# Optimization experiments

Hardware: AMD Instinct MI355X
Metric: run time of the kernel (lower is better)

Reference implementation:

```python
import jax, jax.numpy as jnp
import numpy as np

CLAMP_MIN, CLAMP_MAX = -3.0, 3.0
RANK = 16


def setup_inputs() -> dict:
    key = jax.random.key(0)
    ks = jax.random.split(key, 8)
    B, N, D, H, R = 8, 4096, 1024, 256, RANK
    s = 0.02  # small weight std so clamp/exp are well-conditioned
    return {
        "query_emb": jax.random.normal(ks[0], (B, D), jnp.float32),
        "context_embs": jax.random.normal(ks[1], (B, N, D), jnp.float32),
        "W1": jax.random.normal(ks[2], (D, H), jnp.float32) * s,
        "b1": jnp.zeros((H,), jnp.float32),
        "Wd": jax.random.normal(ks[3], (H, D), jnp.float32) * s,
        "bd": jnp.zeros((D,), jnp.float32),
        "WL": jax.random.normal(ks[4], (H, D * R), jnp.float32) * s,
        "bL": jnp.zeros((D * R,), jnp.float32),
        "Wdel": jax.random.normal(ks[5], (H, D), jnp.float32) * s,
        "bdel": jnp.zeros((D,), jnp.float32),
        "Wa": jax.random.normal(ks[6], (H, D), jnp.float32) * s,
        "ba": jnp.zeros((D,), jnp.float32),
    }


def reference(query_emb, context_embs, W1, b1, Wd, bd, WL, bL, Wdel, bdel, Wa, ba):
    B, N, D = context_embs.shape
    R = RANK
    # Backbone: Linear + ReLU (assumed MLP backbone)
    h = jax.nn.relu(query_emb @ W1 + b1)                      # (B,H)
    # Parameter heads (SkewGaussian.forward)
    log_d = jnp.clip(h @ Wd + bd, CLAMP_MIN, CLAMP_MAX)       # (B,D)
    L = (h @ WL + bL).reshape(B, D, R) * 0.1                  # (B,D,R)
    delta = (h @ Wdel + bdel) * 0.1                           # (B,D)
    alpha = h @ Wa + ba                                       # (B,D)

    mu = query_emb + delta                                    # (B,D)
    diff = context_embs - mu[:, None, :]                      # (B,N,D)
    d_inv = jnp.exp(-log_d)                                   # (B,D)

    # Diagonal Mahalanobis term
    mahal_diag = jnp.einsum('bnd,bd->bn', diff * diff, d_inv) # (B,N)

    # Woodbury correction with small RxR system per batch
    DinvL = d_inv[:, :, None] * L                             # (B,D,R)
    M = jnp.eye(R, dtype=L.dtype)[None] + jnp.einsum('bdr,bds->brs', L, DinvL)  # (B,R,R)
    M_inv = jnp.linalg.inv(M)
    v = diff * d_inv[:, None, :]                              # (B,N,D)
    w = jnp.einsum('bdr,bnd->brn', L, v)                      # (B,R,N)
    correction = jnp.sum(w * jnp.einsum('brs,bsn->brn', M_inv, w), axis=1)  # (B,N)

    mahal = mahal_diag - correction
    log_det = jnp.sum(log_d, axis=-1, keepdims=True) + jnp.linalg.slogdet(M)[1][:, None]  # (B,1)
    symmetric_score = -0.5 * (mahal + log_det)                # (B,N)

    skew_input = jnp.einsum('bd,bnd->bn', alpha, diff)
    skew_score = jax.nn.log_sigmoid(skew_input)
    return symmetric_score + skew_score
```

## Files before the change

### kernel.cpp

```cpp
#include <hip/hip_runtime.h>
#include <math.h>

#define BB 8
#define NN 4096
#define DD 1024
#define HH 256
#define RR 16

#define WS_GT      0
#define WS_MU      131072
#define WS_DINV    139264
#define WS_ALPHA   147456
#define WS_HP      155648
#define WS_LDP     163840
#define WS_M       163968
#define WS_MINV    166016
#define WS_LOGDET  168064
#define WS_L       168080

__global__ __launch_bounds__(256) void ka1_h(
    const float* __restrict__ qe, const float* __restrict__ W1, float* __restrict__ ws)
{
    const int b = blockIdx.x >> 2;
    const int sl = blockIdx.x & 3;
    const int c = threadIdx.x;
    __shared__ float qe_s[256];
    qe_s[c] = qe[b * DD + sl * 256 + c];
    __syncthreads();
    float a0 = 0.f, a1 = 0.f, a2 = 0.f, a3 = 0.f;
    const float* W1p = W1 + (sl * 256) * HH;
    for (int dl = 0; dl < 256; dl += 4) {
        a0 = fmaf(qe_s[dl + 0], W1p[(dl + 0) * HH + c], a0);
        a1 = fmaf(qe_s[dl + 1], W1p[(dl + 1) * HH + c], a1);
        a2 = fmaf(qe_s[dl + 2], W1p[(dl + 2) * HH + c], a2);
        a3 = fmaf(qe_s[dl + 3], W1p[(dl + 3) * HH + c], a3);
    }
    ws[WS_HP + (b * 4 + sl) * HH + c] = (a0 + a1) + (a2 + a3);
}

__global__ __launch_bounds__(256) void ka2_heads(
    const float* __restrict__ qe, const float* __restrict__ b1,
    const float* __restrict__ Wd, const float* __restrict__ bd,
    const float* __restrict__ WL, const float* __restrict__ bL,
    const float* __restrict__ Wdel, const float* __restrict__ bdel,
    const float* __restrict__ Wa, const float* __restrict__ ba,
    float* __restrict__ ws)
{
    __shared__ float h_s[BB * HH];
    __shared__ float red[4][512];
    const int tid = threadIdx.x;

    for (int i = tid; i < BB * HH; i += 256) {
        const int bb = i >> 8, c = i & 255;
        const float v = ws[WS_HP + (bb * 4 + 0) * HH + c] + ws[WS_HP + (bb * 4 + 1) * HH + c]
                      + ws[WS_HP + (bb * 4 + 2) * HH + c] + ws[WS_HP + (bb * 4 + 3) * HH + c]
                      + b1[c];
        h_s[i] = fmaxf(v, 0.f);
    }
    __syncthreads();

    const int blk = blockIdx.x;
    const int lane = tid & 63;
    const int u = tid >> 6;

    int mode; const float* W; const float* bias; int base;
    if (blk < 16)       { mode = 0; W = Wd;   bias = bd;   base = 0;  }
    else if (blk < 32)  { mode = 1; W = Wdel; bias = bdel; base = 16; }
    else if (blk < 48)  { mode = 2; W = Wa;   bias = ba;   base = 32; }
    else                { mode = 3; W = WL;   bias = bL;   base = 48; }
    const int ld = (mode == 3) ? (DD * RR) : DD;
    const int cc = (blk - base) * 64 + lane;

    float acc[8];
    #pragma unroll
    for (int b = 0; b < 8; ++b) acc[b] = 0.f;

    #pragma unroll 4
    for (int rr = 0; rr < 64; ++rr) {
        const int r = u * 64 + rr;
        const float wv = W[r * ld + cc];
        #pragma unroll
        for (int b = 0; b < 8; ++b) acc[b] = fmaf(h_s[b * HH + r], wv, acc[b]);
    }
    #pragma unroll
    for (int b = 0; b < 8; ++b) red[u][lane * 8 + b] = acc[b];
    __syncthreads();

    for (int e = tid; e < 512; e += 256) {
        const int cl = e >> 3, bb = e & 7;
        const int cm = (blk - base) * 64 + cl;
        float s = red[0][e] + red[1][e] + red[2][e] + red[3][e] + bias[cm];
        if (mode == 0) {
            const float ldv = fminf(fmaxf(s, -3.f), 3.f);
            ws[WS_DINV + bb * DD + cm] = expf(-ldv);
            red[0][e] = ldv;
        } else if (mode == 1) {
            ws[WS_MU + bb * DD + cm] = qe[bb * DD + cm] + 0.1f * s;
        } else if (mode == 2) {
            ws[WS_ALPHA + bb * DD + cm] = s;
        } else {
            ws[WS_L + bb * (DD * RR) + cm] = 0.1f * s;
        }
    }
    if (mode == 0) {
        __syncthreads();
        if (tid < 8) {
            float s = 0.f;
            for (int cl = 0; cl < 64; ++cl) s += red[0][cl * 8 + tid];
            ws[WS_LDP + blk * 8 + tid] = s;
        }
    }
}

__global__ __launch_bounds__(256) void kg_gt(float* __restrict__ ws)
{
    const int idx = blockIdx.x * 256 + threadIdx.x;
    const int d = idx & (DD - 1);
    const int r = (idx >> 10) & (RR - 1);
    const int b = idx >> 14;
    ws[WS_GT + idx] = ws[WS_DINV + b * DD + d] * ws[WS_L + (b * DD + d) * RR + r];
}

__global__ __launch_bounds__(256) void kM(float* __restrict__ ws)
{
    const int b = blockIdx.x >> 4;
    const int g = blockIdx.x & 15;
    const int tid = threadIdx.x;
    const int s = tid & 15, dg = tid >> 4;

    const float* Gt = ws + WS_GT + (size_t)b * (RR * DD) + g * DD;
    const float* Lp = ws + WS_L + (size_t)b * (DD * RR);

    float acc = 0.f;
    #pragma unroll 4
    for (int k = 0; k < 64; ++k) {
        const int d = dg * 64 + k;
        acc = fmaf(Gt[d], Lp[d * 16 + s], acc);
    }
    __shared__ float red2[16][17];
    red2[dg][s] = acc;
    __syncthreads();
    if (tid < 16) {
        float m = (tid == g) ? 1.f : 0.f;
        #pragma unroll
        for (int d2 = 0; d2 < 16; ++d2) m += red2[d2][tid];
        ws[WS_M + b * 256 + g * 16 + tid] = m;
    }
}

__global__ __launch_bounds__(256) void kGJ(float* __restrict__ ws)
{
    const int b = blockIdx.x;
    const int tid = threadIdx.x;
    const int i = tid >> 4, j = tid & 15;
    __shared__ float A[16][33];

    A[i][j] = ws[WS_M + b * 256 + i * 16 + j];
    A[i][j + 16] = (i == j) ? 1.f : 0.f;
    __syncthreads();

    float logdetM = 0.f;
    for (int k = 0; k < 16; ++k) {
        const float piv = A[k][k];
        if (tid == 0) logdetM += logf(piv);
        __syncthreads();
        if (i == k) {
            const float rinv = 1.f / piv;
            A[i][j] *= rinv;
            A[i][j + 16] *= rinv;
        }
        __syncthreads();
        const float f = (i == k) ? 0.f : A[i][k];
        __syncthreads();
        if (i != k) {
            A[i][j]      = fmaf(-f, A[k][j],      A[i][j]);
            A[i][j + 16] = fmaf(-f, A[k][j + 16], A[i][j + 16]);
        }
        __syncthreads();
    }
    ws[WS_MINV + b * 256 + i * 16 + j] = A[i][j + 16];
    if (tid == 0) {
        float lds = 0.f;
        for (int k = 0; k < 16; ++k) lds += ws[WS_LDP + k * 8 + b];
        ws[WS_LOGDET + b] = lds + logdetM;
    }
}

__global__ __launch_bounds__(512, 4) void kc_main(
    const float* __restrict__ ctx, const float* __restrict__ ws, float* __restrict__ out)
{
    const int bid = blockIdx.x;
    const int b = bid >> 7;
    const int tile = bid & 127;
    const int wave = threadIdx.x >> 6;
    const int lane = threadIdx.x & 63;
    const int n0 = tile * 32 + wave * 4;

    __shared__ float gt_s[RR * DD];
    {
        float4* gs4 = (float4*)gt_s;
        const float4* Gt4g = (const float4*)(ws + WS_GT + (size_t)b * (RR * DD));
        for (int i = threadIdx.x; i < RR * DD / 4; i += 512) gs4[i] = Gt4g[i];
    }
    __syncthreads();
    const float4* gs4 = (const float4*)gt_s;

    const float4* mu4 = (const float4*)(ws + WS_MU + b * DD);
    const float4* dv4 = (const float4*)(ws + WS_DINV + b * DD);
    const float4* al4 = (const float4*)(ws + WS_ALPHA + b * DD);
    const float4* ctx4 = (const float4*)(ctx + ((size_t)(b * NN + n0)) * DD);

    float g[4][16];
    float md[4], aa[4];
    #pragma unroll
    for (int i = 0; i < 4; ++i) {
        md[i] = 0.f; aa[i] = 0.f;
        #pragma unroll
        for (int r = 0; r < 16; ++r) g[i][r] = 0.f;
    }

    #pragma unroll
    for (int step = 0; step < 4; ++step) {
        const int fi = step * 64 + lane;
        const float4 mv = mu4[fi], dvv = dv4[fi], av = al4[fi];
        const float4 c0 = ctx4[0 * (DD / 4) + fi];
        const float4 c1 = ctx4[1 * (DD / 4) + fi];
        const float4 c2 = ctx4[2 * (DD / 4) + fi];
        const float4 c3 = ctx4[3 * (DD / 4) + fi];

        float diff[4][4];
        diff[0][0] = c0.x - mv.x; diff[0][1] = c0.y - mv.y; diff[0][2] = c0.z - mv.z; diff[0][3] = c0.w - mv.w;
        diff[1][0] = c1.x - mv.x; diff[1][1] = c1.y - mv.y; diff[1][2] = c1.z - mv.z; diff[1][3] = c1.w - mv.w;
        diff[2][0] = c2.x - mv.x; diff[2][1] = c2.y - mv.y; diff[2][2] = c2.z - mv.z; diff[2][3] = c2.w - mv.w;
        diff[3][0] = c3.x - mv.x; diff[3][1] = c3.y - mv.y; diff[3][2] = c3.z - mv.z; diff[3][3] = c3.w - mv.w;

        const float dva[4] = {dvv.x, dvv.y, dvv.z, dvv.w};
        const float ava[4] = {av.x, av.y, av.z, av.w};
        #pragma unroll
        for (int i = 0; i < 4; ++i) {
            #pragma unroll
            for (int j = 0; j < 4; ++j) {
                md[i] = fmaf(diff[i][j] * dva[j], diff[i][j], md[i]);
                aa[i] = fmaf(ava[j], diff[i][j], aa[i]);
            }
        }

        #pragma unroll
        for (int r = 0; r < 16; ++r) {
            const float4 gt = gs4[r * 256 + fi];
            #pragma unroll
            for (int i = 0; i < 4; ++i) {
                g[i][r] = fmaf(gt.x, diff[i][0], g[i][r]);
                g[i][r] = fmaf(gt.y, diff[i][1], g[i][r]);
                g[i][r] = fmaf(gt.z, diff[i][2], g[i][r]);
                g[i][r] = fmaf(gt.w, diff[i][3], g[i][r]);
            }
        }
    }

    float v[64];
    #pragma unroll
    for (int i = 0; i < 4; ++i)
        #pragma unroll
        for (int r = 0; r < 16; ++r) v[i * 16 + r] = g[i][r];

    #pragma unroll
    for (int s6 = 0; s6 < 6; ++s6) {
        const int m = 1 << s6;
        const int half = 32 >> s6;
        const bool up = (lane & m) != 0;
        #pragma unroll
        for (int ii = 0; ii < half; ++ii) {
            float x0 = v[2 * ii], x1 = v[2 * ii + 1];
            float y0 = __shfl_xor(x0, m, 64);
            float y1 = __shfl_xor(x1, m, 64);
            v[ii] = up ? (x1 + y1) : (x0 + y0);
        }
    }
    const float w = v[0];

    #pragma unroll
    for (int m = 1; m < 64; m <<= 1) {
        #pragma unroll
        for (int i = 0; i < 4; ++i) {
            md[i] += __shfl_xor(md[i], m, 64);
            aa[i] += __shfl_xor(aa[i], m, 64);
        }
    }

    const int r = lane & 15;
    const int rowbase = lane & 48;
    const float* Minv = ws + WS_MINV + b * 256 + r * 16;
    float y = 0.f;
    #pragma unroll
    for (int s = 0; s < 16; ++s) y = fmaf(Minv[s], __shfl(w, rowbase + s, 64), y);
    float corr = w * y;
    corr += __shfl_xor(corr, 1, 64);
    corr += __shfl_xor(corr, 2, 64);
    corr += __shfl_xor(corr, 4, 64);
    corr += __shfl_xor(corr, 8, 64);

    const float ld = ws[WS_LOGDET + b];
    if ((lane & 15) == 0) {
        const int i = lane >> 4;
        const float mdv = (i & 2) ? ((i & 1) ? md[3] : md[2]) : ((i & 1) ? md[1] : md[0]);
        const float aav = (i & 2) ? ((i & 1) ? aa[3] : aa[2]) : ((i & 1) ? aa[1] : aa[0]);
        const float lsig = fminf(aav, 0.f) - log1pf(expf(-fabsf(aav)));
        out[(size_t)b * NN + n0 + i] = -0.5f * (mdv - corr + ld) + lsig;
    }
}

extern "C" void kernel_launch(void* const* d_in, const int* in_sizes, int n_in,
                              void* d_out, int out_size, void* d_ws, size_t ws_size,
                              hipStream_t stream)
{
    const float* qe   = (const float*)d_in[0];
    const float* ctx  = (const float*)d_in[1];
    const float* W1   = (const float*)d_in[2];
    const float* b1   = (const float*)d_in[3];
    const float* Wd   = (const float*)d_in[4];
    const float* bd   = (const float*)d_in[5];
    const float* WL   = (const float*)d_in[6];
    const float* bL   = (const float*)d_in[7];
    const float* Wdel = (const float*)d_in[8];
    const float* bdel = (const float*)d_in[9];
    const float* Wa   = (const float*)d_in[10];
    const float* ba   = (const float*)d_in[11];
    float* out = (float*)d_out;
    float* ws  = (float*)d_ws;

    ka1_h<<<32, 256, 0, stream>>>(qe, W1, ws);
    ka2_heads<<<304, 256, 0, stream>>>(qe, b1, Wd, bd, WL, bL, Wdel, bdel, Wa, ba, ws);
    kg_gt<<<512, 256, 0, stream>>>(ws);
    kM<<<128, 256, 0, stream>>>(ws);
    kGJ<<<8, 256, 0, stream>>>(ws);
    kc_main<<<1024, 512, 0, stream>>>(ctx, ws, out);
}
```

Before: 326.2 us.

## Split W1 GEMV finer, fuse M build with Gauss-Jordan, relax main kernel occupancy

Spreads the backbone GEMV across 128 blocks instead of 32 by splitting the input dimension into 16 slices, so each block does less serial work. Merges the M-matrix reduction and the Gauss-Jordan inversion into one 1024-thread kernel per batch, removing a launch and a global round trip. The main context kernel drops its occupancy hint from 4 to 2 blocks per CU, partially unrolls the step loop, and defers the d_inv/alpha loads to shorten register live ranges. The fused kernel runs only 8 blocks doing serial loops, and lower occupancy in the bandwidth-bound main kernel could hurt latency hiding.

```diff
diff --git a/kernel.cpp b/kernel.cpp
--- a/kernel.cpp
+++ b/kernel.cpp
@@ -12,30 +12,30 @@
 #define WS_DINV    139264
 #define WS_ALPHA   147456
 #define WS_HP      155648
-#define WS_LDP     163840
-#define WS_M       163968
-#define WS_MINV    166016
-#define WS_LOGDET  168064
-#define WS_L       168080
+#define WS_LDP     188416
+#define WS_MINV    188544
+#define WS_LOGDET  190592
+#define WS_L       190608
 
 __global__ __launch_bounds__(256) void ka1_h(
     const float* __restrict__ qe, const float* __restrict__ W1, float* __restrict__ ws)
 {
-    const int b = blockIdx.x >> 2;
-    const int sl = blockIdx.x & 3;
+    const int b = blockIdx.x >> 4;
+    const int sl = blockIdx.x & 15;
     const int c = threadIdx.x;
-    __shared__ float qe_s[256];
-    qe_s[c] = qe[b * DD + sl * 256 + c];
+    __shared__ float qe_s[64];
+    if (c < 64) qe_s[c] = qe[b * DD + sl * 64 + c];
     __syncthreads();
     float a0 = 0.f, a1 = 0.f, a2 = 0.f, a3 = 0.f;
-    const float* W1p = W1 + (sl * 256) * HH;
-    for (int dl = 0; dl < 256; dl += 4) {
+    const float* W1p = W1 + (sl * 64) * HH;
+    #pragma unroll 4
+    for (int dl = 0; dl < 64; dl += 4) {
         a0 = fmaf(qe_s[dl + 0], W1p[(dl + 0) * HH + c], a0);
         a1 = fmaf(qe_s[dl + 1], W1p[(dl + 1) * HH + c], a1);
         a2 = fmaf(qe_s[dl + 2], W1p[(dl + 2) * HH + c], a2);
         a3 = fmaf(qe_s[dl + 3], W1p[(dl + 3) * HH + c], a3);
     }
-    ws[WS_HP + (b * 4 + sl) * HH + c] = (a0 + a1) + (a2 + a3);
+    ws[WS_HP + (b * 16 + sl) * HH + c] = (a0 + a1) + (a2 + a3);
 }
 
 __global__ __launch_bounds__(256) void ka2_heads(
@@ -52,9 +52,9 @@
 
     for (int i = tid; i < BB * HH; i += 256) {
         const int bb = i >> 8, c = i & 255;
-        const float v = ws[WS_HP + (bb * 4 + 0) * HH + c] + ws[WS_HP + (bb * 4 + 1) * HH + c]
-                      + ws[WS_HP + (bb * 4 + 2) * HH + c] + ws[WS_HP + (bb * 4 + 3) * HH + c]
-                      + b1[c];
+        float v = b1[c];
+        #pragma unroll
+        for (int k = 0; k < 16; ++k) v += ws[WS_HP + (bb * 16 + k) * HH + c];
         h_s[i] = fmaxf(v, 0.f);
     }
     __syncthreads();
@@ -121,42 +121,34 @@
     ws[WS_GT + idx] = ws[WS_DINV + b * DD + d] * ws[WS_L + (b * DD + d) * RR + r];
 }
 
-__global__ __launch_bounds__(256) void kM(float* __restrict__ ws)
-{
-    const int b = blockIdx.x >> 4;
-    const int g = blockIdx.x & 15;
-    const int tid = threadIdx.x;
-    const int s = tid & 15, dg = tid >> 4;
-
-    const float* Gt = ws + WS_GT + (size_t)b * (RR * DD) + g * DD;
-    const float* Lp = ws + WS_L + (size_t)b * (DD * RR);
-
-    float acc = 0.f;
-    #pragma unroll 4
-    for (int k = 0; k < 64; ++k) {
-        const int d = dg * 64 + k;
-        acc = fmaf(Gt[d], Lp[d * 16 + s], acc);
-    }
-    __shared__ float red2[16][17];
-    red2[dg][s] = acc;
-    __syncthreads();
-    if (tid < 16) {
-        float m = (tid == g) ? 1.f : 0.f;
-        #pragma unroll
-        for (int d2 = 0; d2 < 16; ++d2) m += red2[d2][tid];
-        ws[WS_M + b * 256 + g * 16 + tid] = m;
-    }
-}
-
-__global__ __launch_bounds__(256) void kGJ(float* __restrict__ ws)
+__global__ __launch_bounds__(1024) void kMGJ(float* __restrict__ ws)
 {
     const int b = blockIdx.x;
     const int tid = threadIdx.x;
-    const int i = tid >> 4, j = tid & 15;
+    const int dgr = tid >> 8;
+    const int gs = tid & 255;
+    const int g = gs >> 4, s = gs & 15;
+
+    const float* Gt = ws + WS_GT + (size_t)b * (RR * DD);
+    const float* Lp = ws + WS_L + (size_t)b * (DD * RR);
+
+    float acc = 0.f;
+    #pragma unroll 8
+    for (int k = 0; k < 256; ++k) {
+        const int d = dgr * 256 + k;
+        acc = fmaf(Gt[g * DD + d], Lp[d * 16 + s], acc);
+    }
+
+    __shared__ float Mp[4][256];
     __shared__ float A[16][33];
-
-    A[i][j] = ws[WS_M + b * 256 + i * 16 + j];
-    A[i][j + 16] = (i == j) ? 1.f : 0.f;
+    Mp[dgr][gs] = acc;
+    __syncthreads();
+
+    const bool act = (tid < 256);
+    if (act) {
+        A[g][s] = ((g == s) ? 1.f : 0.f) + Mp[0][gs] + Mp[1][gs] + Mp[2][gs] + Mp[3][gs];
+        A[g][s + 16] = (g == s) ? 1.f : 0.f;
+    }
     __syncthreads();
 
     float logdetM = 0.f;
@@ -164,21 +156,21 @@
         const float piv = A[k][k];
         if (tid == 0) logdetM += logf(piv);
         __syncthreads();
-        if (i == k) {
+        if (act && g == k) {
             const float rinv = 1.f / piv;
-            A[i][j] *= rinv;
-            A[i][j + 16] *= rinv;
-        }
-        __syncthreads();
-        const float f = (i == k) ? 0.f : A[i][k];
-        __syncthreads();
-        if (i != k) {
-            A[i][j]      = fmaf(-f, A[k][j],      A[i][j]);
-            A[i][j + 16] = fmaf(-f, A[k][j + 16], A[i][j + 16]);
-        }
-        __syncthreads();
-    }
-    ws[WS_MINV + b * 256 + i * 16 + j] = A[i][j + 16];
+            A[g][s] *= rinv;
+            A[g][s + 16] *= rinv;
+        }
+        __syncthreads();
+        const float f = (act && g != k) ? A[g][k] : 0.f;
+        __syncthreads();
+        if (act && g != k) {
+            A[g][s]      = fmaf(-f, A[k][s],      A[g][s]);
+            A[g][s + 16] = fmaf(-f, A[k][s + 16], A[g][s + 16]);
+        }
+        __syncthreads();
+    }
+    if (act) ws[WS_MINV + b * 256 + g * 16 + s] = A[g][s + 16];
     if (tid == 0) {
         float lds = 0.f;
         for (int k = 0; k < 16; ++k) lds += ws[WS_LDP + k * 8 + b];
@@ -186,7 +178,7 @@
     }
 }
 
-__global__ __launch_bounds__(512, 4) void kc_main(
+__global__ __launch_bounds__(512, 2) void kc_main(
     const float* __restrict__ ctx, const float* __restrict__ ws, float* __restrict__ out)
 {
     const int bid = blockIdx.x;
@@ -219,14 +211,14 @@
         for (int r = 0; r < 16; ++r) g[i][r] = 0.f;
     }
 
-    #pragma unroll
+    #pragma unroll 2
     for (int step = 0; step < 4; ++step) {
         const int fi = step * 64 + lane;
-        const float4 mv = mu4[fi], dvv = dv4[fi], av = al4[fi];
         const float4 c0 = ctx4[0 * (DD / 4) + fi];
         const float4 c1 = ctx4[1 * (DD / 4) + fi];
         const float4 c2 = ctx4[2 * (DD / 4) + fi];
         const float4 c3 = ctx4[3 * (DD / 4) + fi];
+        const float4 mv = mu4[fi];
 
         float diff[4][4];
         diff[0][0] = c0.x - mv.x; diff[0][1] = c0.y - mv.y; diff[0][2] = c0.z - mv.z; diff[0][3] = c0.w - mv.w;
@@ -234,14 +226,18 @@
         diff[2][0] = c2.x - mv.x; diff[2][1] = c2.y - mv.y; diff[2][2] = c2.z - mv.z; diff[2][3] = c2.w - mv.w;
         diff[3][0] = c3.x - mv.x; diff[3][1] = c3.y - mv.y; diff[3][2] = c3.z - mv.z; diff[3][3] = c3.w - mv.w;
 
-        const float dva[4] = {dvv.x, dvv.y, dvv.z, dvv.w};
-        const float ava[4] = {av.x, av.y, av.z, av.w};
-        #pragma unroll
-        for (int i = 0; i < 4; ++i) {
+        {
+            const float4 dvv = dv4[fi];
+            const float4 av = al4[fi];
+            const float dva[4] = {dvv.x, dvv.y, dvv.z, dvv.w};
+            const float ava[4] = {av.x, av.y, av.z, av.w};
             #pragma unroll
-            for (int j = 0; j < 4; ++j) {
-                md[i] = fmaf(diff[i][j] * dva[j], diff[i][j], md[i]);
-                aa[i] = fmaf(ava[j], diff[i][j], aa[i]);
+            for (int i = 0; i < 4; ++i) {
+                #pragma unroll
+                for (int j = 0; j < 4; ++j) {
+                    md[i] = fmaf(diff[i][j] * dva[j], diff[i][j], md[i]);
+                    aa[i] = fmaf(ava[j], diff[i][j], aa[i]);
+                }
             }
         }
 
@@ -329,10 +325,9 @@
     float* out = (float*)d_out;
     float* ws  = (float*)d_ws;
 
-    ka1_h<<<32, 256, 0, stream>>>(qe, W1, ws);
+    ka1_h<<<128, 256, 0, stream>>>(qe, W1, ws);
     ka2_heads<<<304, 256, 0, stream>>>(qe, b1, Wd, bd, WL, bL, Wdel, bdel, Wa, ba, ws);
     kg_gt<<<512, 256, 0, stream>>>(ws);
-    kM<<<128, 256, 0, stream>>>(ws);
-    kGJ<<<8, 256, 0, stream>>>(ws);
+    kMGJ<<<8, 1024, 0, stream>>>(ws);
     kc_main<<<1024, 512, 0, stream>>>(ctx, ws, out);
 }
```

Measured after the change: 285.8 us. 12.4% less time.
